# Kernel tuning notes

Measured on AMD Instinct MI355X. Metric: run time of the kernel, lower is better.

Reference implementation:

```python
import jax, jax.numpy as jnp
import numpy as np

N, A, OBS, H, E, ITERS = 2000, 16, 64, 128, 16000, 8


def _init_linear(key, din, dout):
    kw, kb = jax.random.split(key)
    s = 1.0 / np.sqrt(din)
    W = jax.random.uniform(kw, (dout, din), minval=-s, maxval=s, dtype=jnp.float32)
    b = jax.random.uniform(kb, (dout,), minval=-s, maxval=s, dtype=jnp.float32)
    return W, b


def setup_inputs() -> dict:
    key = jax.random.key(0)
    ks = jax.random.split(key, 20)
    x = jax.random.normal(ks[0], (N, OBS), dtype=jnp.float32)
    prev_action = jax.random.normal(ks[1], (N, A), dtype=jnp.float32)
    state = jax.random.normal(ks[2], (1, N, H), dtype=jnp.float32)
    # edges: unique-ish random pairs with i < j (no self loops)
    rng = np.random.default_rng(0)
    ei = rng.integers(0, N - 1, size=E)
    ej = rng.integers(ei + 1, N)
    edges = jnp.asarray(np.stack([ei, ej], axis=1), dtype=jnp.int32)
    # GRU params (torch layout: rows = [r; z; n])
    s = 1.0 / np.sqrt(H)
    gru_wih = jax.random.uniform(ks[3], (3 * H, OBS + A), minval=-s, maxval=s, dtype=jnp.float32)
    gru_whh = jax.random.uniform(ks[4], (3 * H, H), minval=-s, maxval=s, dtype=jnp.float32)
    gru_bih = jax.random.uniform(ks[5], (3 * H,), minval=-s, maxval=s, dtype=jnp.float32)
    gru_bhh = jax.random.uniform(ks[6], (3 * H,), minval=-s, maxval=s, dtype=jnp.float32)
    # utility MLP: [H, 256, 256, A]
    uW0, ub0 = _init_linear(ks[7], H, 256)
    uW1, ub1 = _init_linear(ks[8], 256, 256)
    uW2, ub2 = _init_linear(ks[9], 256, A)
    # payoff MLP: [2H, H, 256, 256, A, A*A]  (faithful to source's dim-list reuse)
    pW0, pb0 = _init_linear(ks[10], 2 * H, H)
    pW1, pb1 = _init_linear(ks[11], H, 256)
    pW2, pb2 = _init_linear(ks[12], 256, 256)
    pW3, pb3 = _init_linear(ks[13], 256, A)
    pW4, pb4 = _init_linear(ks[14], A, A * A)
    return dict(x=x, prev_action=prev_action, state=state, edges=edges,
                gru_wih=gru_wih, gru_whh=gru_whh, gru_bih=gru_bih, gru_bhh=gru_bhh,
                uW0=uW0, ub0=ub0, uW1=uW1, ub1=ub1, uW2=uW2, ub2=ub2,
                pW0=pW0, pb0=pb0, pW1=pW1, pb1=pb1, pW2=pW2, pb2=pb2,
                pW3=pW3, pb3=pb3, pW4=pW4, pb4=pb4)


def _mlp(x, params):
    n = len(params)
    for i, (W, b) in enumerate(params):
        x = x @ W.T + b
        if i < n - 1:
            x = jax.nn.relu(x)
    return x


def _gru_step(inp, h, wih, whh, bih, bhh):
    gi = inp @ wih.T + bih          # [N, 3H]
    gh = h @ whh.T + bhh            # [N, 3H]
    gir, giz, gin = jnp.split(gi, 3, axis=-1)
    ghr, ghz, ghn = jnp.split(gh, 3, axis=-1)
    r = jax.nn.sigmoid(gir + ghr)
    z = jax.nn.sigmoid(giz + ghz)
    n = jnp.tanh(gin + r * ghn)
    return (1.0 - z) * n + z * h


def _message_passing(u, p, ei, ej):
    """u: [N,A] differentiable, p: [E,A,A] differentiable.
    Messages are computed under stop_gradient (torch.no_grad in source);
    Q of the per-iteration greedy action is differentiable in u, p."""
    u_sg = jax.lax.stop_gradient(u)
    p_sg = jax.lax.stop_gradient(p)
    node_idx = jnp.arange(N)
    edge_idx = jnp.arange(E)

    def step(carry, _):
        M, q_max, opt_a = carry            # M[recv, send, A]
        S = M.sum(axis=1)                  # [N, A] total incoming per node
        base_i = u_sg[ei] + S[ei] - M[ei, ej]   # [E, A] indexed by a_i
        base_j = u_sg[ej] + S[ej] - M[ej, ei]   # [E, A] indexed by a_j
        # message i -> j: max over a_i of (p[e,ai,aj] + base_i[ai])
        msg_to_j = (p_sg + base_i[:, :, None]).max(axis=1)   # [E, A]
        msg_to_j = msg_to_j - msg_to_j.mean(axis=-1, keepdims=True)
        # message j -> i (source reduces over dim 0 = a_i; replicated faithfully)
        msg_to_i = (p_sg + base_j[:, None, :]).max(axis=1)   # [E, A]
        msg_to_i = msg_to_i - msg_to_i.mean(axis=-1, keepdims=True)
        M = M.at[ej, ei].set(msg_to_j).at[ei, ej].set(msg_to_i)
        # greedy action per node
        a_idx = jnp.argmax(u_sg + M.sum(axis=1), axis=-1)    # [N]
        q_real = u[node_idx, a_idx].sum() + p[edge_idx, a_idx[ei], a_idx[ej]].sum()
        better = q_real > q_max
        q_max = jnp.where(better, q_real, q_max)
        a_onehot = jax.nn.one_hot(a_idx, A, dtype=u.dtype)
        opt_a = jnp.where(better, a_onehot, opt_a)
        return (M, q_max, opt_a), None

    M0 = jnp.zeros((N, N, A), dtype=u.dtype)
    q0 = jnp.zeros((), dtype=u.dtype)
    a0 = jnp.zeros((N, A), dtype=u.dtype)
    (M, q_max, opt_a), _ = jax.lax.scan(step, (M0, q0, a0), None, length=ITERS)
    return opt_a, q_max


def reference(x, prev_action, state, edges,
              gru_wih, gru_whh, gru_bih, gru_bhh,
              uW0, ub0, uW1, ub1, uW2, ub2,
              pW0, pb0, pW1, pb1, pW2, pb2, pW3, pb3, pW4, pb4):
    ei, ej = edges[:, 0], edges[:, 1]
    enc_in = jnp.concatenate([x, prev_action], axis=-1)        # [N, OBS+A]
    h = _gru_step(enc_in, state[0], gru_wih, gru_whh, gru_bih, gru_bhh)  # [N, H]
    state_out = h.reshape(1, 1, N, H)
    u_params = [(uW0, ub0), (uW1, ub1), (uW2, ub2)]
    p_params = [(pW0, pb0), (pW1, pb1), (pW2, pb2), (pW3, pb3), (pW4, pb4)]
    u = _mlp(h, u_params) / N                                  # [N, A]
    s_ij = jnp.concatenate([h[ei], h[ej]], axis=-1)            # [E, 2H]
    s_ji = jnp.concatenate([h[ej], h[ei]], axis=-1)
    p_ij = _mlp(s_ij, p_params).reshape(E, A, A) / E
    p_ji = _mlp(s_ji, p_params).reshape(E, A, A) / E
    p = 0.5 * (p_ij + p_ji)                                    # [E, A, A]
    a, q_max = _message_passing(u, p, ei, ej)
    return (a, q_max, u[None], p, state_out)
```

## Files before the change

### kernel.cpp

```cpp
#include <hip/hip_runtime.h>
#include <math.h>

#define N_NODES 2000
#define NA 16
#define NOBS 64
#define NH 128
#define NE 16000
#define NITERS 8

#define WS_MSG       0
#define WS_FLAGS     300000
#define WS_Q         512000
#define WS_SBUF      512016
#define WS_AIDX      800016
#define WS_W         816016
#define WS_PT        832016
#define WS_GIT       (WS_PT + 4000000)
#define WS_GHT       (WS_GIT + 30720)
#define WS_WB        4928016
#define WS_UW0T      (WS_WB + 0)
#define WS_UWCAT     (WS_WB + 32768)
#define WS_UW1T      (WS_WB + 65536)
#define WS_UW2T      (WS_WB + 131072)
#define WS_CAB       (WS_WB + 241664)

#define F16_W1H 0
#define F16_W1L 32768
#define F16_W2H 65536
#define F16_W2L 131072
#define F16_W3H 196608
#define F16_W3L 200704
#define F16_W4H 204800
#define F16_W4L 212992

#define NBLK 500

typedef _Float16 half8 __attribute__((ext_vector_type(8)));
typedef float f32x4 __attribute__((ext_vector_type(4)));

__global__ __launch_bounds__(256) void setup_kernel(
    float* __restrict__ ws, const int* __restrict__ edges,
    const float* __restrict__ uW0, const float* __restrict__ uW1,
    const float* __restrict__ uW2, const float* __restrict__ pW0,
    const float* __restrict__ pW1, const float* __restrict__ pW2,
    const float* __restrict__ pW3, const float* __restrict__ pW4,
    const float* __restrict__ gwih, const float* __restrict__ gwhh)
{
    if (blockIdx.x >= 1024) {
        int e = (blockIdx.x - 1024) * 256 + threadIdx.x;
        if (e < NE) {
            int i = edges[2 * e], j = edges[2 * e + 1];
            ((int*)(ws + WS_PT))[i * N_NODES + j] = -1;
        }
        return;
    }
    const int total = 341904;
    for (int idx = blockIdx.x * 256 + threadIdx.x; idx < total;
         idx += 1024 * 256) {
        if (idx < 16) {
            ws[WS_Q + idx] = 0.f;
        } else {
            int t = idx - 16;
            if (t < 135168) {
                float v;
                if (t < 32768) {
                    int k = t / 256, o = t % 256;
                    v = uW0[o * 128 + k];
                } else if (t < 65536) {
                    int q = t - 32768, k = q / 256, o = q % 256;
                    v = (o < 128) ? pW0[o * 256 + k]
                                  : pW0[(o - 128) * 256 + 128 + k];
                } else if (t < 131072) {
                    int q = t - 65536, k = q / 256, o = q % 256;
                    v = uW1[o * 256 + k];
                } else {
                    int q = t - 131072, k = q / 16, o = q % 16;
                    v = uW2[o * 256 + k];
                }
                ws[WS_WB + t] = v;
            } else if (t < 215056) {
                int q = t - 135168;
                if (q < 30720) {
                    int k4 = q / 1536, r = q % 1536, g = r >> 2, c = r & 3;
                    ws[WS_GIT + q] = gwih[g * 80 + 4 * k4 + c];
                } else if (q < 79872) {
                    int q2 = q - 30720;
                    int k4 = q2 / 1536, r = q2 % 1536, g = r >> 2, c = r & 3;
                    ws[WS_GHT + q2] = gwhh[g * 128 + 4 * k4 + c];
                }
            } else if (t < 325648) {
                int q = t - 215056;
                if (q >= 110592) continue;
                _Float16* fw = (_Float16*)ws;
                float v; int hoff, loff;
                if (q < 32768) {
                    v = pW1[q]; hoff = F16_W1H + q; loff = F16_W1L + q;
                } else if (q < 98304) {
                    int z = q - 32768; v = pW2[z];
                    hoff = F16_W2H + z; loff = F16_W2L + z;
                } else if (q < 102400) {
                    int z = q - 98304; v = pW3[z];
                    hoff = F16_W3H + z; loff = F16_W3L + z;
                } else {
                    int z = q - 102400; int n = z >> 5, kk = z & 31;
                    v = (kk < 16) ? pW4[n * 16 + kk] : 0.f;
                    hoff = F16_W4H + z; loff = F16_W4L + z;
                }
                _Float16 hv = (_Float16)v;
                fw[hoff] = hv;
                fw[loff] = (_Float16)(v - (float)hv);
            } else {
                int qf = t - 325648;
                ((int*)(ws + WS_FLAGS))[qf] = 0;
            }
        }
    }
}

__global__ __launch_bounds__(256) void gru_kernel(
    const float* __restrict__ x, const float* __restrict__ pa,
    const float* __restrict__ st, const float* __restrict__ wihT,
    const float* __restrict__ whhT, const float* __restrict__ bih,
    const float* __restrict__ bhh, float* __restrict__ h_out,
    const int* __restrict__ edges, int* __restrict__ owner)
{
    if (blockIdx.x >= 250) {
        int e = (blockIdx.x - 250) * 256 + threadIdx.x;
        if (e < NE) {
            int i = edges[2 * e], j = edges[2 * e + 1];
            atomicMax(&owner[i * N_NODES + j], e);
        }
        return;
    }
    __shared__ float enc[8][80];
    __shared__ float hp[8][128];
    __shared__ float gi[8][384];
    __shared__ float gh[8][384];
    const int tid = threadIdx.x;
    const int n0 = blockIdx.x * 8;

    for (int idx = tid; idx < 8 * 80; idx += 256) {
        int r = idx / 80, c = idx % 80;
        enc[r][c] = (c < 64) ? x[(n0 + r) * 64 + c] : pa[(n0 + r) * 16 + (c - 64)];
    }
    for (int idx = tid; idx < 8 * 128; idx += 256) {
        int r = idx >> 7, c = idx & 127;
        hp[r][c] = st[(n0 + r) * 128 + c];
    }
    __syncthreads();

    for (int idx = tid; idx < 8 * 384; idx += 256) {
        int g = idx % 384, r = idx / 384;
        float s1 = bih[g];
        #pragma unroll 5
        for (int k4 = 0; k4 < 20; ++k4) {
            const float4 ev = *(const float4*)&enc[r][4 * k4];
            const float4 wv = *(const float4*)&wihT[k4 * 1536 + g * 4];
            s1 = fmaf(ev.x, wv.x, fmaf(ev.y, wv.y, fmaf(ev.z, wv.z, fmaf(ev.w, wv.w, s1))));
        }
        gi[r][g] = s1;
        float s2 = bhh[g];
        #pragma unroll 8
        for (int k4 = 0; k4 < 32; ++k4) {
            const float4 hv = *(const float4*)&hp[r][4 * k4];
            const float4 wv = *(const float4*)&whhT[k4 * 1536 + g * 4];
            s2 = fmaf(hv.x, wv.x, fmaf(hv.y, wv.y, fmaf(hv.z, wv.z, fmaf(hv.w, wv.w, s2))));
        }
        gh[r][g] = s2;
    }
    __syncthreads();

    for (int idx = tid; idx < 8 * 128; idx += 256) {
        int r = idx >> 7, c = idx & 127;
        float rr = 1.f / (1.f + expf(-(gi[r][c] + gh[r][c])));
        float zz = 1.f / (1.f + expf(-(gi[r][128 + c] + gh[r][128 + c])));
        float nn = tanhf(gi[r][256 + c] + rr * gh[r][256 + c]);
        h_out[(n0 + r) * 128 + c] = (1.f - zz) * nn + zz * hp[r][c];
    }
}

__global__ __launch_bounds__(256) void umlp_kernel(
    const float* __restrict__ h, const float* __restrict__ w0t,
    const float* __restrict__ b0, const float* __restrict__ w1t,
    const float* __restrict__ b1, const float* __restrict__ w2t,
    const float* __restrict__ b2, const float* __restrict__ wcat,
    float* __restrict__ u_out, float* __restrict__ Sbuf,
    float* __restrict__ cab, const int* __restrict__ edges,
    const int* __restrict__ owner, int* __restrict__ wflag)
{
    if (blockIdx.x >= 500) {
        int e = (blockIdx.x - 500) * 256 + threadIdx.x;
        if (e < NE) {
            int i = edges[2 * e], j = edges[2 * e + 1];
            wflag[e] = (owner[i * N_NODES + j] == e) ? 1 : 0;
        }
        return;
    }
    __shared__ float A[8][128];
    __shared__ float B[8][256];
    const int tid = threadIdx.x;
    const bool is_cab = blockIdx.x >= 250;
    const int n0 = (is_cab ? blockIdx.x - 250 : blockIdx.x) * 8;

    for (int idx = tid; idx < 8 * 128; idx += 256) {
        int r = idx >> 7, c = idx & 127;
        A[r][c] = h[(n0 + r) * 128 + c];
    }
    __syncthreads();

    if (is_cab) {
        const int o = tid;
        const float* wp = wcat + o;
        float wA[4], wB[4];
        #pragma unroll
        for (int c = 0; c < 4; ++c) wA[c] = wp[c * 256];
        float acc[8];
        #pragma unroll
        for (int r = 0; r < 8; ++r) acc[r] = 0.f;
        for (int k4 = 0; k4 < 32; k4 += 2) {
            #pragma unroll
            for (int c = 0; c < 4; ++c) wB[c] = wp[(4 * (k4 + 1) + c) * 256];
            #pragma unroll
            for (int r = 0; r < 8; ++r) {
                const float4 av = *(const float4*)&A[r][4 * k4];
                acc[r] = fmaf(av.x, wA[0], fmaf(av.y, wA[1], fmaf(av.z, wA[2], fmaf(av.w, wA[3], acc[r]))));
            }
            #pragma unroll
            for (int c = 0; c < 4; ++c) wA[c] = wp[(4 * (k4 + 2) + c) * 256];
            #pragma unroll
            for (int r = 0; r < 8; ++r) {
                const float4 av = *(const float4*)&A[r][4 * k4 + 4];
                acc[r] = fmaf(av.x, wB[0], fmaf(av.y, wB[1], fmaf(av.z, wB[2], fmaf(av.w, wB[3], acc[r]))));
            }
        }
        #pragma unroll
        for (int r = 0; r < 8; ++r) cab[(n0 + r) * 256 + o] = acc[r];
        return;
    }

    {
        const int o = tid;
        const float* wp = w0t + o;
        float wA[4], wB[4];
        #pragma unroll
        for (int c = 0; c < 4; ++c) wA[c] = wp[c * 256];
        float acc[8];
        #pragma unroll
        for (int r = 0; r < 8; ++r) acc[r] = b0[o];
        for (int k4 = 0; k4 < 32; k4 += 2) {
            #pragma unroll
            for (int c = 0; c < 4; ++c) wB[c] = wp[(4 * (k4 + 1) + c) * 256];
            #pragma unroll
            for (int r = 0; r < 8; ++r) {
                const float4 av = *(const float4*)&A[r][4 * k4];
                acc[r] = fmaf(av.x, wA[0], fmaf(av.y, wA[1], fmaf(av.z, wA[2], fmaf(av.w, wA[3], acc[r]))));
            }
            #pragma unroll
            for (int c = 0; c < 4; ++c) wA[c] = wp[(4 * (k4 + 2) + c) * 256];
            #pragma unroll
            for (int r = 0; r < 8; ++r) {
                const float4 av = *(const float4*)&A[r][4 * k4 + 4];
                acc[r] = fmaf(av.x, wB[0], fmaf(av.y, wB[1], fmaf(av.z, wB[2], fmaf(av.w, wB[3], acc[r]))));
            }
        }
        #pragma unroll
        for (int r = 0; r < 8; ++r) B[r][o] = fmaxf(acc[r], 0.f);
    }
    __syncthreads();
    {
        const int o = tid;
        const float* wp = w1t + o;
        float wA[4], wB[4];
        #pragma unroll
        for (int c = 0; c < 4; ++c) wA[c] = wp[c * 256];
        float acc[8];
        #pragma unroll
        for (int r = 0; r < 8; ++r) acc[r] = b1[o];
        for (int k4 = 0; k4 < 64; k4 += 2) {
            #pragma unroll
            for (int c = 0; c < 4; ++c) wB[c] = wp[(4 * (k4 + 1) + c) * 256];
            #pragma unroll
            for (int r = 0; r < 8; ++r) {
                const float4 av = *(const float4*)&B[r][4 * k4];
                acc[r] = fmaf(av.x, wA[0], fmaf(av.y, wA[1], fmaf(av.z, wA[2], fmaf(av.w, wA[3], acc[r]))));
            }
            #pragma unroll
            for (int c = 0; c < 4; ++c) wA[c] = wp[(4 * (k4 + 2) + c) * 256];
            #pragma unroll
            for (int r = 0; r < 8; ++r) {
                const float4 av = *(const float4*)&B[r][4 * k4 + 4];
                acc[r] = fmaf(av.x, wB[0], fmaf(av.y, wB[1], fmaf(av.z, wB[2], fmaf(av.w, wB[3], acc[r]))));
            }
        }
        __syncthreads();
        #pragma unroll
        for (int r = 0; r < 8; ++r) B[r][o] = fmaxf(acc[r], 0.f);
    }
    __syncthreads();
    if (tid < 128) {
        int r = tid >> 4, o = tid & 15;
        float acc = b2[o];
        for (int k4 = 0; k4 < 64; ++k4) {
            const float4 av = *(const float4*)&B[r][4 * k4];
            acc = fmaf(av.x, w2t[(4 * k4 + 0) * 16 + o],
                  fmaf(av.y, w2t[(4 * k4 + 1) * 16 + o],
                  fmaf(av.z, w2t[(4 * k4 + 2) * 16 + o],
                  fmaf(av.w, w2t[(4 * k4 + 3) * 16 + o], acc))));
        }
        float val = acc * (1.f / N_NODES);
        int idx = (n0 + r) * 16 + o;
        u_out[idx] = val;
        #pragma unroll
        for (int t = 0; t < NITERS + 1; ++t) Sbuf[t * 32000 + idx] = val;
    }
}

__device__ __forceinline__ void grid_bar(int* flags, int gval)
{
    int* gen8 = flags + NBLK * 32;
    __syncthreads();
    if (blockIdx.x == 0) {
        const int i = threadIdx.x;
        if (i >= 1 && i < NBLK) {
            while (__hip_atomic_load(&flags[i * 32], __ATOMIC_RELAXED,
                                     __HIP_MEMORY_SCOPE_AGENT) < gval)
                __builtin_amdgcn_s_sleep(2);
        }
        __syncthreads();
        if (i < 8)
            __hip_atomic_store(&gen8[i * 32], gval, __ATOMIC_RELAXED,
                               __HIP_MEMORY_SCOPE_AGENT);
    } else {
        if (threadIdx.x == 0) {
            asm volatile("s_waitcnt vmcnt(0)" ::: "memory");
            __hip_atomic_store(&flags[blockIdx.x * 32], gval, __ATOMIC_RELAXED,
                               __HIP_MEMORY_SCOPE_AGENT);
            while (__hip_atomic_load(&gen8[(blockIdx.x & 7) * 32],
                                     __ATOMIC_RELAXED,
                                     __HIP_MEMORY_SCOPE_AGENT) < gval)
                __builtin_amdgcn_s_sleep(2);
        }
        __syncthreads();
    }
}

__global__ __launch_bounds__(512, 4) void pmlp_mp_kernel(
    const float* __restrict__ cab, const int* __restrict__ edges,
    const float* __restrict__ b0, const _Float16* __restrict__ fw,
    const float* __restrict__ b1, const float* __restrict__ b2,
    const float* __restrict__ b3, const float* __restrict__ b4,
    float* __restrict__ p_out, const float* __restrict__ u,
    float* __restrict__ Sbuf, const int* __restrict__ wflag,
    int* __restrict__ aidx, float* __restrict__ q,
    float* __restrict__ a_out, float* __restrict__ q_out,
    int* __restrict__ flags)
{
    __shared__ __align__(16) _Float16 Ah[64][264];
    __shared__ __align__(16) _Float16 Al[64][264];
    __shared__ float C16[64][16];
    __shared__ int fi[64], se[64];

    const int tid  = threadIdx.x;
    const int bid  = blockIdx.x;
    const int e0   = bid * 32;
    const int wid  = tid >> 6;
    const int lane = tid & 63;
    const int lrow = lane & 15;
    const int lgrp = lane >> 4;
    const int koff = 8 * lgrp;

    if (tid < 32) {
        int i = edges[2 * (e0 + tid)], j = edges[2 * (e0 + tid) + 1];
        fi[2 * tid] = i;     se[2 * tid] = j;
        fi[2 * tid + 1] = j; se[2 * tid + 1] = i;
    }
    __syncthreads();

    {
        const int cl = tid & 127;
        const int rh = tid >> 7;
        const float bb = b0[cl];
        #pragma unroll 4
        for (int r = rh * 16; r < rh * 16 + 16; ++r) {
            float v = cab[fi[r] * 256 + cl] + cab[se[r] * 256 + 128 + cl] + bb;
            v = fmaxf(v, 0.f);
            _Float16 hv = (_Float16)v;
            Ah[r][cl] = hv;
            Al[r][cl] = (_Float16)(v - (float)hv);
        }
    }
    __syncthreads();

    f32x4 acc[4][2];

    #pragma unroll
    for (int mt = 0; mt < 4; ++mt)
        #pragma unroll
        for (int nt = 0; nt < 2; ++nt) acc[mt][nt] = (f32x4){0.f, 0.f, 0.f, 0.f};
    #pragma unroll
    for (int ks = 0; ks < 4; ++ks) {
        half8 ah[4], al[4];
        #pragma unroll
        for (int mt = 0; mt < 4; ++mt) {
            ah[mt] = *(const half8*)&Ah[16 * mt + lrow][32 * ks + koff];
            al[mt] = *(const half8*)&Al[16 * mt + lrow][32 * ks + koff];
        }
        #pragma unroll
        for (int nt = 0; nt < 2; ++nt) {
            const int n = 32 * wid + 16 * nt + lrow;
            half8 bh = *(const half8*)(fw + F16_W1H + n * 128 + 32 * ks + koff);
            half8 bl = *(const half8*)(fw + F16_W1L + n * 128 + 32 * ks + koff);
            #pragma unroll
            for (int mt = 0; mt < 4; ++mt) {
                acc[mt][nt] = __builtin_amdgcn_mfma_f32_16x16x32_f16(ah[mt], bh, acc[mt][nt], 0, 0, 0);
                acc[mt][nt] = __builtin_amdgcn_mfma_f32_16x16x32_f16(ah[mt], bl, acc[mt][nt], 0, 0, 0);
                acc[mt][nt] = __builtin_amdgcn_mfma_f32_16x16x32_f16(al[mt], bh, acc[mt][nt], 0, 0, 0);
            }
        }
    }
    __syncthreads();
    #pragma unroll
    for (int nt = 0; nt < 2; ++nt) {
        const int col = 32 * wid + 16 * nt + lrow;
        const float bv = b1[col];
        #pragma unroll
        for (int mt = 0; mt < 4; ++mt) {
            #pragma unroll
            for (int r = 0; r < 4; ++r) {
                const int row = 16 * mt + 4 * lgrp + r;
                float v = fmaxf(acc[mt][nt][r] + bv, 0.f);
                _Float16 hv = (_Float16)v;
                Ah[row][col] = hv;
                Al[row][col] = (_Float16)(v - (float)hv);
            }
        }
    }
    __syncthreads();

    #pragma unroll
    for (int mt = 0; mt < 4; ++mt)
        #pragma unroll
        for (int nt = 0; nt < 2; ++nt) acc[mt][nt] = (f32x4){0.f, 0.f, 0.f, 0.f};
    for (int ks = 0; ks < 8; ++ks) {
        half8 ah[4], al[4];
        #pragma unroll
        for (int mt = 0; mt < 4; ++mt) {
            ah[mt] = *(const half8*)&Ah[16 * mt + lrow][32 * ks + koff];
            al[mt] = *(const half8*)&Al[16 * mt + lrow][32 * ks + koff];
        }
        #pragma unroll
        for (int nt = 0; nt < 2; ++nt) {
            const int n = 32 * wid + 16 * nt + lrow;
            half8 bh = *(const half8*)(fw + F16_W2H + n * 256 + 32 * ks + koff);
            half8 bl = *(const half8*)(fw + F16_W2L + n * 256 + 32 * ks + koff);
            #pragma unroll
            for (int mt = 0; mt < 4; ++mt) {
                acc[mt][nt] = __builtin_amdgcn_mfma_f32_16x16x32_f16(ah[mt], bh, acc[mt][nt], 0, 0, 0);
                acc[mt][nt] = __builtin_amdgcn_mfma_f32_16x16x32_f16(ah[mt], bl, acc[mt][nt], 0, 0, 0);
                acc[mt][nt] = __builtin_amdgcn_mfma_f32_16x16x32_f16(al[mt], bh, acc[mt][nt], 0, 0, 0);
            }
        }
    }
    __syncthreads();
    #pragma unroll
    for (int nt = 0; nt < 2; ++nt) {
        const int col = 32 * wid + 16 * nt + lrow;
        const float bv = b2[col];
        #pragma unroll
        for (int mt = 0; mt < 4; ++mt) {
            #pragma unroll
            for (int r = 0; r < 4; ++r) {
                const int row = 16 * mt + 4 * lgrp + r;
                float v = fmaxf(acc[mt][nt][r] + bv, 0.f);
                _Float16 hv = (_Float16)v;
                Ah[row][col] = hv;
                Al[row][col] = (_Float16)(v - (float)hv);
            }
        }
    }
    __syncthreads();

    if (wid < 4) {
        f32x4 acc3 = {0.f, 0.f, 0.f, 0.f};
        #pragma unroll
        for (int ks = 0; ks < 8; ++ks) {
            half8 ah = *(const half8*)&Ah[16 * wid + lrow][32 * ks + koff];
            half8 al = *(const half8*)&Al[16 * wid + lrow][32 * ks + koff];
            half8 bh = *(const half8*)(fw + F16_W3H + lrow * 256 + 32 * ks + koff);
            half8 bl = *(const half8*)(fw + F16_W3L + lrow * 256 + 32 * ks + koff);
            acc3 = __builtin_amdgcn_mfma_f32_16x16x32_f16(ah, bh, acc3, 0, 0, 0);
            acc3 = __builtin_amdgcn_mfma_f32_16x16x32_f16(ah, bl, acc3, 0, 0, 0);
            acc3 = __builtin_amdgcn_mfma_f32_16x16x32_f16(al, bh, acc3, 0, 0, 0);
        }
        const float b3v = b3[lrow];
        #pragma unroll
        for (int r = 0; r < 4; ++r)
            C16[16 * wid + 4 * lgrp + r][lrow] = fmaxf(acc3[r] + b3v, 0.f);
    }
    __syncthreads();

    float* pTl = (float*)Ah;

    {
        half8 a4h[4], a4l[4];
        #pragma unroll
        for (int mt = 0; mt < 4; ++mt) {
            half8 hh, ll;
            #pragma unroll
            for (int j = 0; j < 8; ++j) { hh[j] = (_Float16)0.f; ll[j] = (_Float16)0.f; }
            if (lgrp < 2) {
                #pragma unroll
                for (int j = 0; j < 8; ++j) {
                    float v = C16[16 * mt + lrow][8 * lgrp + j];
                    _Float16 hv = (_Float16)v;
                    hh[j] = hv;
                    ll[j] = (_Float16)(v - (float)hv);
                }
            }
            a4h[mt] = hh; a4l[mt] = ll;
        }
        #pragma unroll
        for (int nt = 0; nt < 2; ++nt) {
            const int o = 32 * wid + 16 * nt + lrow;
            const float b4v = b4[o];
            half8 bh = *(const half8*)(fw + F16_W4H + o * 32 + koff);
            half8 bl = *(const half8*)(fw + F16_W4L + o * 32 + koff);
            const int ot = (o & 15) * 16 + (o >> 4);
            #pragma unroll
            for (int mt = 0; mt < 4; ++mt) {
                f32x4 a4 = {0.f, 0.f, 0.f, 0.f};
                a4 = __builtin_amdgcn_mfma_f32_16x16x32_f16(a4h[mt], bh, a4, 0, 0, 0);
                a4 = __builtin_amdgcn_mfma_f32_16x16x32_f16(a4h[mt], bl, a4, 0, 0, 0);
                a4 = __builtin_amdgcn_mfma_f32_16x16x32_f16(a4l[mt], bh, a4, 0, 0, 0);
                const int s0 = 8 * mt + 2 * lgrp;
                float pa = (0.5f * (a4[0] + a4[1]) + b4v) * (1.f / NE);
                float pb = (0.5f * (a4[2] + a4[3]) + b4v) * (1.f / NE);
                __hip_atomic_store(&p_out[(e0 + s0) * 256 + o], pa,
                                   __ATOMIC_RELAXED, __HIP_MEMORY_SCOPE_AGENT);
                __hip_atomic_store(&p_out[(e0 + s0 + 1) * 256 + o], pb,
                                   __ATOMIC_RELAXED, __HIP_MEMORY_SCOPE_AGENT);
                pTl[s0 * 256 + ot] = pa;
                pTl[(s0 + 1) * 256 + ot] = pb;
            }
        }
    }
    __syncthreads();

    const int g = tid >> 4;
    const int L = tid & 15;
    const int e = e0 + g;
    const int gi = edges[2 * e], gj = edges[2 * e + 1];
    const int wf = wflag[e];
    float pv[16];
    #pragma unroll
    for (int a4i = 0; a4i < 4; ++a4i) {
        float4 v = *(const float4*)&pTl[g * 256 + L * 16 + 4 * a4i];
        pv[4 * a4i + 0] = v.x; pv[4 * a4i + 1] = v.y;
        pv[4 * a4i + 2] = v.z; pv[4 * a4i + 3] = v.w;
    }
    float vmax = -INFINITY;
    #pragma unroll
    for (int a = 0; a < 16; ++a) vmax = fmaxf(vmax, pv[a]);
    float mold_ij = 0.f, mold_ji = 0.f;

    for (int t = 0; t < NITERS; ++t) {
        const float* uSo = Sbuf + t * 32000;
        float* uSn = Sbuf + (t + 1) * 32000;
        const float bi = uSo[gi * 16 + L] - mold_ij;
        const float bj = uSo[gj * 16 + L] - mold_ji;
        float mj = -INFINITY;
        #pragma unroll
        for (int a = 0; a < 16; ++a)
            mj = fmaxf(mj, pv[a] + __shfl(bi, a, 16));
        float mi = vmax + bj;
        float sj = mj, si = mi;
        #pragma unroll
        for (int off = 1; off < 16; off <<= 1) {
            sj += __shfl_xor(sj, off, 16);
            si += __shfl_xor(si, off, 16);
        }
        mj -= sj * (1.f / 16.f);
        mi -= si * (1.f / 16.f);
        mold_ji = mj;
        mold_ij = mi;
        if (wf) {
            atomicAdd(&uSn[gj * 16 + L], mj);
            atomicAdd(&uSn[gi * 16 + L], mi);
        }
        grid_bar(flags, t + 1);
    }

    if (bid < 288) {
        const int t2 = bid / 36;
        const int r2 = (bid % 36) * 512 + tid;
        const float* Sn = Sbuf + (t2 + 1) * 32000;
        float partial = 0.f;
        if (r2 < N_NODES) {
            int n = r2;
            float bv = Sn[n * 16];
            int best = 0;
            #pragma unroll
            for (int a = 1; a < 16; ++a) {
                float v = Sn[n * 16 + a];
                if (v > bv) { bv = v; best = a; }
            }
            __hip_atomic_store(&aidx[t2 * N_NODES + n], best, __ATOMIC_RELAXED,
                               __HIP_MEMORY_SCOPE_AGENT);
            partial = u[n * 16 + best];
        } else if (r2 < N_NODES + NE) {
            int ee = r2 - N_NODES;
            int ii = edges[2 * ee], jj = edges[2 * ee + 1];
            float bvi = Sn[ii * 16]; int ai = 0;
            #pragma unroll
            for (int a = 1; a < 16; ++a) {
                float v = Sn[ii * 16 + a];
                if (v > bvi) { bvi = v; ai = a; }
            }
            float bvj = Sn[jj * 16]; int aj = 0;
            #pragma unroll
            for (int a = 1; a < 16; ++a) {
                float v = Sn[jj * 16 + a];
                if (v > bvj) { bvj = v; aj = a; }
            }
            partial = p_out[ee * 256 + ai * 16 + aj];
        }
        #pragma unroll
        for (int off = 1; off < 64; off <<= 1)
            partial += __shfl_xor(partial, off, 64);
        if ((tid & 63) == 0) atomicAdd(&q[t2], partial);
    }
    grid_bar(flags, NITERS + 1);

    const int r = bid * 512 + tid;
    if (r < N_NODES * 16) {
        float cur = 0.f; int best_t = -1;
        #pragma unroll
        for (int t2 = 0; t2 < NITERS; ++t2) {
            float qv = q[t2];
            if (qv > cur) { cur = qv; best_t = t2; }
        }
        int n = r >> 4, c = r & 15;
        float val = 0.f;
        if (best_t >= 0 && aidx[best_t * N_NODES + n] == c) val = 1.f;
        a_out[r] = val;
        if (r == 0) q_out[0] = cur;
    }
}

extern "C" void kernel_launch(void* const* d_in, const int* in_sizes, int n_in,
                              void* d_out, int out_size, void* d_ws, size_t ws_size,
                              hipStream_t stream)
{
    (void)in_sizes; (void)n_in; (void)out_size; (void)ws_size;
    const float* x    = (const float*)d_in[0];
    const float* pa   = (const float*)d_in[1];
    const float* st   = (const float*)d_in[2];
    const int*   edges= (const int*)d_in[3];
    const float* gwih = (const float*)d_in[4];
    const float* gwhh = (const float*)d_in[5];
    const float* gbih = (const float*)d_in[6];
    const float* gbhh = (const float*)d_in[7];
    const float* uW0 = (const float*)d_in[8];  const float* ub0 = (const float*)d_in[9];
    const float* uW1 = (const float*)d_in[10]; const float* ub1 = (const float*)d_in[11];
    const float* uW2 = (const float*)d_in[12]; const float* ub2 = (const float*)d_in[13];
    const float* pW0 = (const float*)d_in[14]; const float* pb0 = (const float*)d_in[15];
    const float* pW1 = (const float*)d_in[16]; const float* pb1 = (const float*)d_in[17];
    const float* pW2 = (const float*)d_in[18]; const float* pb2 = (const float*)d_in[19];
    const float* pW3 = (const float*)d_in[20]; const float* pb3 = (const float*)d_in[21];
    const float* pW4 = (const float*)d_in[22]; const float* pb4 = (const float*)d_in[23];

    float* out   = (float*)d_out;
    float* a_out = out;
    float* q_out = out + 32000;
    float* u_out = out + 32001;
    float* p_out = out + 64001;
    float* h_out = out + 4160001;

    float* ws   = (float*)d_ws;
    float* Sbuf = ws + WS_SBUF;
    float* q    = ws + WS_Q;
    int*   flg  = (int*)(ws + WS_FLAGS);
    int*   aidx = (int*)(ws + WS_AIDX);
    int*   wfl  = (int*)(ws + WS_W);
    float* cab  = ws + WS_CAB;
    int*   owner= (int*)(ws + WS_PT);

    setup_kernel<<<1087, 256, 0, stream>>>(ws, edges, uW0, uW1, uW2,
                                           pW0, pW1, pW2, pW3, pW4, gwih, gwhh);
    gru_kernel<<<313, 256, 0, stream>>>(x, pa, st, ws + WS_GIT, ws + WS_GHT,
                                        gbih, gbhh, h_out, edges, owner);
    umlp_kernel<<<563, 256, 0, stream>>>(h_out, ws + WS_UW0T, ub0,
                                         ws + WS_UW1T, ub1, ws + WS_UW2T, ub2,
                                         ws + WS_UWCAT, u_out, Sbuf, cab,
                                         edges, owner, wfl);
    pmlp_mp_kernel<<<NBLK, 512, 0, stream>>>(cab, edges, pb0,
                                             (const _Float16*)ws,
                                             pb1, pb2, pb3, pb4, p_out,
                                             u_out, Sbuf, wfl, aidx, q,
                                             a_out, q_out, flg);
}
```

Baseline: 266.1 us.

## Fuse GRU and utility MLP stages into persistent kernel with grid barriers

Removes the separate GRU and utility-MLP kernels and folds their work into the persistent message-passing kernel. Each of the 500 blocks now handles 4 nodes, and grid-wide barriers replace the kernel boundaries between the GRU, the MLP/cab stage and the payoff stage. Edge ownership flags are kept in shared memory instead of a global array. This saves two launches and the gaps between them, but adds two grid barriers and spreads the small GEMMs over fewer rows per block, which costs weight reuse.

```diff
diff --git a/kernel.cpp b/kernel.cpp
--- a/kernel.cpp
+++ b/kernel.cpp
@@ -37,6 +37,8 @@
 
 typedef _Float16 half8 __attribute__((ext_vector_type(8)));
 typedef float f32x4 __attribute__((ext_vector_type(4)));
+
+#define AGST(p, v) __hip_atomic_store((p), (v), __ATOMIC_RELAXED, __HIP_MEMORY_SCOPE_AGENT)
 
 __global__ __launch_bounds__(256) void setup_kernel(
     float* __restrict__ ws, const int* __restrict__ edges,
@@ -117,204 +119,6 @@
     }
 }
 
-__global__ __launch_bounds__(256) void gru_kernel(
-    const float* __restrict__ x, const float* __restrict__ pa,
-    const float* __restrict__ st, const float* __restrict__ wihT,
-    const float* __restrict__ whhT, const float* __restrict__ bih,
-    const float* __restrict__ bhh, float* __restrict__ h_out,
-    const int* __restrict__ edges, int* __restrict__ owner)
-{
-    if (blockIdx.x >= 250) {
-        int e = (blockIdx.x - 250) * 256 + threadIdx.x;
-        if (e < NE) {
-            int i = edges[2 * e], j = edges[2 * e + 1];
-            atomicMax(&owner[i * N_NODES + j], e);
-        }
-        return;
-    }
-    __shared__ float enc[8][80];
-    __shared__ float hp[8][128];
-    __shared__ float gi[8][384];
-    __shared__ float gh[8][384];
-    const int tid = threadIdx.x;
-    const int n0 = blockIdx.x * 8;
-
-    for (int idx = tid; idx < 8 * 80; idx += 256) {
-        int r = idx / 80, c = idx % 80;
-        enc[r][c] = (c < 64) ? x[(n0 + r) * 64 + c] : pa[(n0 + r) * 16 + (c - 64)];
-    }
-    for (int idx = tid; idx < 8 * 128; idx += 256) {
-        int r = idx >> 7, c = idx & 127;
-        hp[r][c] = st[(n0 + r) * 128 + c];
-    }
-    __syncthreads();
-
-    for (int idx = tid; idx < 8 * 384; idx += 256) {
-        int g = idx % 384, r = idx / 384;
-        float s1 = bih[g];
-        #pragma unroll 5
-        for (int k4 = 0; k4 < 20; ++k4) {
-            const float4 ev = *(const float4*)&enc[r][4 * k4];
-            const float4 wv = *(const float4*)&wihT[k4 * 1536 + g * 4];
-            s1 = fmaf(ev.x, wv.x, fmaf(ev.y, wv.y, fmaf(ev.z, wv.z, fmaf(ev.w, wv.w, s1))));
-        }
-        gi[r][g] = s1;
-        float s2 = bhh[g];
-        #pragma unroll 8
-        for (int k4 = 0; k4 < 32; ++k4) {
-            const float4 hv = *(const float4*)&hp[r][4 * k4];
-            const float4 wv = *(const float4*)&whhT[k4 * 1536 + g * 4];
-            s2 = fmaf(hv.x, wv.x, fmaf(hv.y, wv.y, fmaf(hv.z, wv.z, fmaf(hv.w, wv.w, s2))));
-        }
-        gh[r][g] = s2;
-    }
-    __syncthreads();
-
-    for (int idx = tid; idx < 8 * 128; idx += 256) {
-        int r = idx >> 7, c = idx & 127;
-        float rr = 1.f / (1.f + expf(-(gi[r][c] + gh[r][c])));
-        float zz = 1.f / (1.f + expf(-(gi[r][128 + c] + gh[r][128 + c])));
-        float nn = tanhf(gi[r][256 + c] + rr * gh[r][256 + c]);
-        h_out[(n0 + r) * 128 + c] = (1.f - zz) * nn + zz * hp[r][c];
-    }
-}
-
-__global__ __launch_bounds__(256) void umlp_kernel(
-    const float* __restrict__ h, const float* __restrict__ w0t,
-    const float* __restrict__ b0, const float* __restrict__ w1t,
-    const float* __restrict__ b1, const float* __restrict__ w2t,
-    const float* __restrict__ b2, const float* __restrict__ wcat,
-    float* __restrict__ u_out, float* __restrict__ Sbuf,
-    float* __restrict__ cab, const int* __restrict__ edges,
-    const int* __restrict__ owner, int* __restrict__ wflag)
-{
-    if (blockIdx.x >= 500) {
-        int e = (blockIdx.x - 500) * 256 + threadIdx.x;
-        if (e < NE) {
-            int i = edges[2 * e], j = edges[2 * e + 1];
-            wflag[e] = (owner[i * N_NODES + j] == e) ? 1 : 0;
-        }
-        return;
-    }
-    __shared__ float A[8][128];
-    __shared__ float B[8][256];
-    const int tid = threadIdx.x;
-    const bool is_cab = blockIdx.x >= 250;
-    const int n0 = (is_cab ? blockIdx.x - 250 : blockIdx.x) * 8;
-
-    for (int idx = tid; idx < 8 * 128; idx += 256) {
-        int r = idx >> 7, c = idx & 127;
-        A[r][c] = h[(n0 + r) * 128 + c];
-    }
-    __syncthreads();
-
-    if (is_cab) {
-        const int o = tid;
-        const float* wp = wcat + o;
-        float wA[4], wB[4];
-        #pragma unroll
-        for (int c = 0; c < 4; ++c) wA[c] = wp[c * 256];
-        float acc[8];
-        #pragma unroll
-        for (int r = 0; r < 8; ++r) acc[r] = 0.f;
-        for (int k4 = 0; k4 < 32; k4 += 2) {
-            #pragma unroll
-            for (int c = 0; c < 4; ++c) wB[c] = wp[(4 * (k4 + 1) + c) * 256];
-            #pragma unroll
-            for (int r = 0; r < 8; ++r) {
-                const float4 av = *(const float4*)&A[r][4 * k4];
-                acc[r] = fmaf(av.x, wA[0], fmaf(av.y, wA[1], fmaf(av.z, wA[2], fmaf(av.w, wA[3], acc[r]))));
-            }
-            #pragma unroll
-            for (int c = 0; c < 4; ++c) wA[c] = wp[(4 * (k4 + 2) + c) * 256];
-            #pragma unroll
-            for (int r = 0; r < 8; ++r) {
-                const float4 av = *(const float4*)&A[r][4 * k4 + 4];
-                acc[r] = fmaf(av.x, wB[0], fmaf(av.y, wB[1], fmaf(av.z, wB[2], fmaf(av.w, wB[3], acc[r]))));
-            }
-        }
-        #pragma unroll
-        for (int r = 0; r < 8; ++r) cab[(n0 + r) * 256 + o] = acc[r];
-        return;
-    }
-
-    {
-        const int o = tid;
-        const float* wp = w0t + o;
-        float wA[4], wB[4];
-        #pragma unroll
-        for (int c = 0; c < 4; ++c) wA[c] = wp[c * 256];
-        float acc[8];
-        #pragma unroll
-        for (int r = 0; r < 8; ++r) acc[r] = b0[o];
-        for (int k4 = 0; k4 < 32; k4 += 2) {
-            #pragma unroll
-            for (int c = 0; c < 4; ++c) wB[c] = wp[(4 * (k4 + 1) + c) * 256];
-            #pragma unroll
-            for (int r = 0; r < 8; ++r) {
-                const float4 av = *(const float4*)&A[r][4 * k4];
-                acc[r] = fmaf(av.x, wA[0], fmaf(av.y, wA[1], fmaf(av.z, wA[2], fmaf(av.w, wA[3], acc[r]))));
-            }
-            #pragma unroll
-            for (int c = 0; c < 4; ++c) wA[c] = wp[(4 * (k4 + 2) + c) * 256];
-            #pragma unroll
-            for (int r = 0; r < 8; ++r) {
-                const float4 av = *(const float4*)&A[r][4 * k4 + 4];
-                acc[r] = fmaf(av.x, wB[0], fmaf(av.y, wB[1], fmaf(av.z, wB[2], fmaf(av.w, wB[3], acc[r]))));
-            }
-        }
-        #pragma unroll
-        for (int r = 0; r < 8; ++r) B[r][o] = fmaxf(acc[r], 0.f);
-    }
-    __syncthreads();
-    {
-        const int o = tid;
-        const float* wp = w1t + o;
-        float wA[4], wB[4];
-        #pragma unroll
-        for (int c = 0; c < 4; ++c) wA[c] = wp[c * 256];
-        float acc[8];
-        #pragma unroll
-        for (int r = 0; r < 8; ++r) acc[r] = b1[o];
-        for (int k4 = 0; k4 < 64; k4 += 2) {
-            #pragma unroll
-            for (int c = 0; c < 4; ++c) wB[c] = wp[(4 * (k4 + 1) + c) * 256];
-            #pragma unroll
-            for (int r = 0; r < 8; ++r) {
-                const float4 av = *(const float4*)&B[r][4 * k4];
-                acc[r] = fmaf(av.x, wA[0], fmaf(av.y, wA[1], fmaf(av.z, wA[2], fmaf(av.w, wA[3], acc[r]))));
-            }
-            #pragma unroll
-            for (int c = 0; c < 4; ++c) wA[c] = wp[(4 * (k4 + 2) + c) * 256];
-            #pragma unroll
-            for (int r = 0; r < 8; ++r) {
-                const float4 av = *(const float4*)&B[r][4 * k4 + 4];
-                acc[r] = fmaf(av.x, wB[0], fmaf(av.y, wB[1], fmaf(av.z, wB[2], fmaf(av.w, wB[3], acc[r]))));
-            }
-        }
-        __syncthreads();
-        #pragma unroll
-        for (int r = 0; r < 8; ++r) B[r][o] = fmaxf(acc[r], 0.f);
-    }
-    __syncthreads();
-    if (tid < 128) {
-        int r = tid >> 4, o = tid & 15;
-        float acc = b2[o];
-        for (int k4 = 0; k4 < 64; ++k4) {
-            const float4 av = *(const float4*)&B[r][4 * k4];
-            acc = fmaf(av.x, w2t[(4 * k4 + 0) * 16 + o],
-                  fmaf(av.y, w2t[(4 * k4 + 1) * 16 + o],
-                  fmaf(av.z, w2t[(4 * k4 + 2) * 16 + o],
-                  fmaf(av.w, w2t[(4 * k4 + 3) * 16 + o], acc))));
-        }
-        float val = acc * (1.f / N_NODES);
-        int idx = (n0 + r) * 16 + o;
-        u_out[idx] = val;
-        #pragma unroll
-        for (int t = 0; t < NITERS + 1; ++t) Sbuf[t * 32000 + idx] = val;
-    }
-}
-
 __device__ __forceinline__ void grid_bar(int* flags, int gval)
 {
     int* gen8 = flags + NBLK * 32;
@@ -344,21 +148,23 @@
     }
 }
 
-__global__ __launch_bounds__(512, 4) void pmlp_mp_kernel(
-    const float* __restrict__ cab, const int* __restrict__ edges,
-    const float* __restrict__ b0, const _Float16* __restrict__ fw,
-    const float* __restrict__ b1, const float* __restrict__ b2,
-    const float* __restrict__ b3, const float* __restrict__ b4,
-    float* __restrict__ p_out, const float* __restrict__ u,
-    float* __restrict__ Sbuf, const int* __restrict__ wflag,
-    int* __restrict__ aidx, float* __restrict__ q,
-    float* __restrict__ a_out, float* __restrict__ q_out,
-    int* __restrict__ flags)
+__global__ __launch_bounds__(512, 4) void mega_kernel(
+    const float* __restrict__ x, const float* __restrict__ pa,
+    const float* __restrict__ st, const float* __restrict__ bih,
+    const float* __restrict__ bhh, const float* __restrict__ ub0,
+    const float* __restrict__ ub1, const float* __restrict__ ub2,
+    const float* __restrict__ b0, const float* __restrict__ b1,
+    const float* __restrict__ b2, const float* __restrict__ b3,
+    const float* __restrict__ b4, const int* __restrict__ edges,
+    float* __restrict__ ws, float* __restrict__ h_out,
+    float* __restrict__ u_out, float* __restrict__ p_out,
+    float* __restrict__ a_out, float* __restrict__ q_out)
 {
     __shared__ __align__(16) _Float16 Ah[64][264];
     __shared__ __align__(16) _Float16 Al[64][264];
     __shared__ float C16[64][16];
     __shared__ int fi[64], se[64];
+    __shared__ int wfl_l[32];
 
     const int tid  = threadIdx.x;
     const int bid  = blockIdx.x;
@@ -369,12 +175,156 @@
     const int lgrp = lane >> 4;
     const int koff = 8 * lgrp;
 
+    float* sm = (float*)&Ah[0][0];
+    int*   flags = (int*)(ws + WS_FLAGS);
+    int*   owner = (int*)(ws + WS_PT);
+    const _Float16* fw = (const _Float16*)ws;
+    float* Sbuf = ws + WS_SBUF;
+    float* q    = ws + WS_Q;
+    int*   aidx = (int*)(ws + WS_AIDX);
+    float* cab  = ws + WS_CAB;
+
     if (tid < 32) {
         int i = edges[2 * (e0 + tid)], j = edges[2 * (e0 + tid) + 1];
         fi[2 * tid] = i;     se[2 * tid] = j;
         fi[2 * tid + 1] = j; se[2 * tid + 1] = i;
     }
-    __syncthreads();
+
+    {
+        float* enc = sm;
+        float* hp  = sm + 320;
+        float* gi  = sm + 832;
+        float* gh  = sm + 2368;
+        float* A   = sm + 3904;
+        const float* wihT = ws + WS_GIT;
+        const float* whhT = ws + WS_GHT;
+        const int n0 = bid * 4;
+
+        if (tid < 320) {
+            int r = tid / 80, c = tid % 80;
+            enc[r * 80 + c] = (c < 64) ? x[(n0 + r) * 64 + c]
+                                       : pa[(n0 + r) * 16 + (c - 64)];
+        }
+        {
+            int r = tid >> 7, c = tid & 127;
+            hp[r * 128 + c] = st[(n0 + r) * 128 + c];
+        }
+        __syncthreads();
+
+        #pragma unroll
+        for (int ii = 0; ii < 3; ++ii) {
+            int idx = ii * 512 + tid;
+            int g = idx % 384, r = idx / 384;
+            float s1 = bih[g];
+            #pragma unroll 5
+            for (int k4 = 0; k4 < 20; ++k4) {
+                const float4 ev = *(const float4*)&enc[r * 80 + 4 * k4];
+                const float4 wv = *(const float4*)&wihT[k4 * 1536 + g * 4];
+                s1 = fmaf(ev.x, wv.x, fmaf(ev.y, wv.y, fmaf(ev.z, wv.z, fmaf(ev.w, wv.w, s1))));
+            }
+            gi[r * 384 + g] = s1;
+            float s2 = bhh[g];
+            #pragma unroll 8
+            for (int k4 = 0; k4 < 32; ++k4) {
+                const float4 hv = *(const float4*)&hp[r * 128 + 4 * k4];
+                const float4 wv = *(const float4*)&whhT[k4 * 1536 + g * 4];
+                s2 = fmaf(hv.x, wv.x, fmaf(hv.y, wv.y, fmaf(hv.z, wv.z, fmaf(hv.w, wv.w, s2))));
+            }
+            gh[r * 384 + g] = s2;
+        }
+        __syncthreads();
+
+        {
+            int r = tid >> 7, c = tid & 127;
+            float rr = 1.f / (1.f + expf(-(gi[r * 384 + c] + gh[r * 384 + c])));
+            float zz = 1.f / (1.f + expf(-(gi[r * 384 + 128 + c] + gh[r * 384 + 128 + c])));
+            float nn = tanhf(gi[r * 384 + 256 + c] + rr * gh[r * 384 + 256 + c]);
+            float hv = (1.f - zz) * nn + zz * hp[r * 128 + c];
+            A[r * 128 + c] = hv;
+            h_out[(n0 + r) * 128 + c] = hv;
+        }
+        if (tid < 32) {
+            int e = e0 + tid;
+            atomicMax(&owner[fi[2 * tid] * N_NODES + se[2 * tid]], e);
+        }
+    }
+    grid_bar(flags, 1);
+
+    {
+        float* A = sm + 3904;
+        float* B = sm + 4416;
+        const int n0 = bid * 4;
+        const int o  = tid & 255;
+        const int r0 = (tid >> 8) * 2;
+
+        {
+            const float* wp = ws + WS_UW0T + o;
+            float a0 = ub0[o], a1 = a0;
+            for (int k4 = 0; k4 < 32; ++k4) {
+                float w0 = wp[(4 * k4 + 0) * 256], w1 = wp[(4 * k4 + 1) * 256];
+                float w2 = wp[(4 * k4 + 2) * 256], w3 = wp[(4 * k4 + 3) * 256];
+                const float4 v0 = *(const float4*)&A[r0 * 128 + 4 * k4];
+                const float4 v1 = *(const float4*)&A[(r0 + 1) * 128 + 4 * k4];
+                a0 = fmaf(v0.x, w0, fmaf(v0.y, w1, fmaf(v0.z, w2, fmaf(v0.w, w3, a0))));
+                a1 = fmaf(v1.x, w0, fmaf(v1.y, w1, fmaf(v1.z, w2, fmaf(v1.w, w3, a1))));
+            }
+            B[r0 * 256 + o] = fmaxf(a0, 0.f);
+            B[(r0 + 1) * 256 + o] = fmaxf(a1, 0.f);
+        }
+        __syncthreads();
+        {
+            const float* wp = ws + WS_UW1T + o;
+            float a0 = ub1[o], a1 = a0;
+            for (int k4 = 0; k4 < 64; ++k4) {
+                float w0 = wp[(4 * k4 + 0) * 256], w1 = wp[(4 * k4 + 1) * 256];
+                float w2 = wp[(4 * k4 + 2) * 256], w3 = wp[(4 * k4 + 3) * 256];
+                const float4 v0 = *(const float4*)&B[r0 * 256 + 4 * k4];
+                const float4 v1 = *(const float4*)&B[(r0 + 1) * 256 + 4 * k4];
+                a0 = fmaf(v0.x, w0, fmaf(v0.y, w1, fmaf(v0.z, w2, fmaf(v0.w, w3, a0))));
+                a1 = fmaf(v1.x, w0, fmaf(v1.y, w1, fmaf(v1.z, w2, fmaf(v1.w, w3, a1))));
+            }
+            __syncthreads();
+            B[r0 * 256 + o] = fmaxf(a0, 0.f);
+            B[(r0 + 1) * 256 + o] = fmaxf(a1, 0.f);
+        }
+        __syncthreads();
+        if (tid < 64) {
+            int r = tid >> 4, oo = tid & 15;
+            const float* w2t = ws + WS_UW2T;
+            float acc = ub2[oo];
+            for (int k4 = 0; k4 < 64; ++k4) {
+                const float4 av = *(const float4*)&B[r * 256 + 4 * k4];
+                acc = fmaf(av.x, w2t[(4 * k4 + 0) * 16 + oo],
+                      fmaf(av.y, w2t[(4 * k4 + 1) * 16 + oo],
+                      fmaf(av.z, w2t[(4 * k4 + 2) * 16 + oo],
+                      fmaf(av.w, w2t[(4 * k4 + 3) * 16 + oo], acc))));
+            }
+            float val = acc * (1.f / N_NODES);
+            int idx = (n0 + r) * 16 + oo;
+            AGST(&u_out[idx], val);
+            #pragma unroll
+            for (int t = 0; t < NITERS + 1; ++t) AGST(&Sbuf[t * 32000 + idx], val);
+        }
+        {
+            const float* wp = ws + WS_UWCAT + o;
+            float a0 = 0.f, a1 = 0.f;
+            for (int k4 = 0; k4 < 32; ++k4) {
+                float w0 = wp[(4 * k4 + 0) * 256], w1 = wp[(4 * k4 + 1) * 256];
+                float w2 = wp[(4 * k4 + 2) * 256], w3 = wp[(4 * k4 + 3) * 256];
+                const float4 v0 = *(const float4*)&A[r0 * 128 + 4 * k4];
+                const float4 v1 = *(const float4*)&A[(r0 + 1) * 128 + 4 * k4];
+                a0 = fmaf(v0.x, w0, fmaf(v0.y, w1, fmaf(v0.z, w2, fmaf(v0.w, w3, a0))));
+                a1 = fmaf(v1.x, w0, fmaf(v1.y, w1, fmaf(v1.z, w2, fmaf(v1.w, w3, a1))));
+            }
+            AGST(&cab[(n0 + r0) * 256 + o], a0);
+            AGST(&cab[(n0 + r0 + 1) * 256 + o], a1);
+        }
+        if (tid < 32) {
+            int e = e0 + tid;
+            wfl_l[tid] = (owner[fi[2 * tid] * N_NODES + se[2 * tid]] == e) ? 1 : 0;
+        }
+    }
+    grid_bar(flags, 2);
 
     {
         const int cl = tid & 127;
@@ -533,14 +483,12 @@
                 a4 = __builtin_amdgcn_mfma_f32_16x16x32_f16(a4h[mt], bl, a4, 0, 0, 0);
                 a4 = __builtin_amdgcn_mfma_f32_16x16x32_f16(a4l[mt], bh, a4, 0, 0, 0);
                 const int s0 = 8 * mt + 2 * lgrp;
-                float pa = (0.5f * (a4[0] + a4[1]) + b4v) * (1.f / NE);
-                float pb = (0.5f * (a4[2] + a4[3]) + b4v) * (1.f / NE);
-                __hip_atomic_store(&p_out[(e0 + s0) * 256 + o], pa,
-                                   __ATOMIC_RELAXED, __HIP_MEMORY_SCOPE_AGENT);
-                __hip_atomic_store(&p_out[(e0 + s0 + 1) * 256 + o], pb,
-                                   __ATOMIC_RELAXED, __HIP_MEMORY_SCOPE_AGENT);
-                pTl[s0 * 256 + ot] = pa;
-                pTl[(s0 + 1) * 256 + ot] = pb;
+                float pav = (0.5f * (a4[0] + a4[1]) + b4v) * (1.f / NE);
+                float pbv = (0.5f * (a4[2] + a4[3]) + b4v) * (1.f / NE);
+                AGST(&p_out[(e0 + s0) * 256 + o], pav);
+                AGST(&p_out[(e0 + s0 + 1) * 256 + o], pbv);
+                pTl[s0 * 256 + ot] = pav;
+                pTl[(s0 + 1) * 256 + ot] = pbv;
             }
         }
     }
@@ -548,9 +496,8 @@
 
     const int g = tid >> 4;
     const int L = tid & 15;
-    const int e = e0 + g;
-    const int gi = edges[2 * e], gj = edges[2 * e + 1];
-    const int wf = wflag[e];
+    const int gi2 = fi[2 * g], gj2 = se[2 * g];
+    const int wf = wfl_l[g];
     float pv[16];
     #pragma unroll
     for (int a4i = 0; a4i < 4; ++a4i) {
@@ -566,8 +513,8 @@
     for (int t = 0; t < NITERS; ++t) {
         const float* uSo = Sbuf + t * 32000;
         float* uSn = Sbuf + (t + 1) * 32000;
-        const float bi = uSo[gi * 16 + L] - mold_ij;
-        const float bj = uSo[gj * 16 + L] - mold_ji;
+        const float bi = uSo[gi2 * 16 + L] - mold_ij;
+        const float bj = uSo[gj2 * 16 + L] - mold_ji;
         float mj = -INFINITY;
         #pragma unroll
         for (int a = 0; a < 16; ++a)
@@ -584,10 +531,10 @@
         mold_ji = mj;
         mold_ij = mi;
         if (wf) {
-            atomicAdd(&uSn[gj * 16 + L], mj);
-            atomicAdd(&uSn[gi * 16 + L], mi);
-        }
-        grid_bar(flags, t + 1);
+            atomicAdd(&uSn[gj2 * 16 + L], mj);
+            atomicAdd(&uSn[gi2 * 16 + L], mi);
+        }
+        grid_bar(flags, 3 + t);
     }
 
     if (bid < 288) {
@@ -604,9 +551,8 @@
                 float v = Sn[n * 16 + a];
                 if (v > bv) { bv = v; best = a; }
             }
-            __hip_atomic_store(&aidx[t2 * N_NODES + n], best, __ATOMIC_RELAXED,
-                               __HIP_MEMORY_SCOPE_AGENT);
-            partial = u[n * 16 + best];
+            AGST(&aidx[t2 * N_NODES + n], best);
+            partial = u_out[n * 16 + best];
         } else if (r2 < N_NODES + NE) {
             int ee = r2 - N_NODES;
             int ii = edges[2 * ee], jj = edges[2 * ee + 1];
@@ -629,7 +575,7 @@
             partial += __shfl_xor(partial, off, 64);
         if ((tid & 63) == 0) atomicAdd(&q[t2], partial);
     }
-    grid_bar(flags, NITERS + 1);
+    grid_bar(flags, NITERS + 3);
 
     const int r = bid * 512 + tid;
     if (r < N_NODES * 16) {
@@ -676,26 +622,13 @@
     float* p_out = out + 64001;
     float* h_out = out + 4160001;
 
-    float* ws   = (float*)d_ws;
-    float* Sbuf = ws + WS_SBUF;
-    float* q    = ws + WS_Q;
-    int*   flg  = (int*)(ws + WS_FLAGS);
-    int*   aidx = (int*)(ws + WS_AIDX);
-    int*   wfl  = (int*)(ws + WS_W);
-    float* cab  = ws + WS_CAB;
-    int*   owner= (int*)(ws + WS_PT);
+    float* ws = (float*)d_ws;
 
     setup_kernel<<<1087, 256, 0, stream>>>(ws, edges, uW0, uW1, uW2,
                                            pW0, pW1, pW2, pW3, pW4, gwih, gwhh);
-    gru_kernel<<<313, 256, 0, stream>>>(x, pa, st, ws + WS_GIT, ws + WS_GHT,
-                                        gbih, gbhh, h_out, edges, owner);
-    umlp_kernel<<<563, 256, 0, stream>>>(h_out, ws + WS_UW0T, ub0,
-                                         ws + WS_UW1T, ub1, ws + WS_UW2T, ub2,
-                                         ws + WS_UWCAT, u_out, Sbuf, cab,
-                                         edges, owner, wfl);
-    pmlp_mp_kernel<<<NBLK, 512, 0, stream>>>(cab, edges, pb0,
-                                             (const _Float16*)ws,
-                                             pb1, pb2, pb3, pb4, p_out,
-                                             u_out, Sbuf, wfl, aidx, q,
-                                             a_out, q_out, flg);
+    mega_kernel<<<NBLK, 512, 0, stream>>>(x, pa, st, gbih, gbhh,
+                                          ub0, ub1, ub2,
+                                          pb0, pb1, pb2, pb3, pb4,
+                                          edges, ws, h_out, u_out, p_out,
+                                          a_out, q_out);
 }
```

Result: no change. 261.5 us (-1.7%).
